# Optimization experiments

Hardware: AMD Instinct MI355X
Metric: run time of the kernel (lower is better)

Reference implementation:

```python
import jax, jax.numpy as jnp
import numpy as np

B, S, D, E = 4, 4096, 2048, 64
NOISE_STD = 1.0


def setup_inputs() -> dict:
    key = jax.random.key(0)
    k1, k2, k3, k4 = jax.random.split(key, 4)
    x = jax.random.normal(k1, (B, S, D), dtype=jnp.float32)
    lim = float(np.sqrt(6.0 / (D + E)))  # glorot_uniform
    W_gate = jax.random.uniform(k2, (D, E), jnp.float32, -lim, lim)
    # keras inits noise_dense kernel to zeros; use tiny random values so the
    # noise path is numerically exercised (zeros would make it trivially ln(2)).
    W_noise = 0.02 * jax.random.normal(k3, (D, E), dtype=jnp.float32)
    noise = jax.random.normal(k4, (B * S, E), dtype=jnp.float32)
    return {"x": x, "W_gate": W_gate, "W_noise": W_noise, "noise": noise, "top_k": 2}


def reference(x, W_gate, W_noise, noise, top_k):
    b, s, d = x.shape
    e = W_gate.shape[1]
    xf = x.reshape(-1, d)                         # [N, D], N = b*s
    gate_logits = xf @ W_gate                     # [N, E]
    # training-mode noise injection
    noise_logits = xf @ W_noise                   # [N, E]
    nstd = jax.nn.softplus(noise_logits) * (NOISE_STD / (e * e))
    gate_logits = gate_logits + noise * nstd
    # top-k mask + masked softmax
    top_vals, top_idx = jax.lax.top_k(gate_logits, top_k)   # [N, K]
    n = gate_logits.shape[0]
    mask = jnp.zeros_like(gate_logits).at[jnp.arange(n)[:, None], top_idx].set(1.0)
    masked_logits = jnp.where(mask > 0, gate_logits, jnp.float32(-1e9))
    expert_weights = jax.nn.softmax(masked_logits, axis=-1)  # [N, E]
    raw_gate_probs = jax.nn.softmax(gate_logits, axis=-1)    # [N, E]
    expert_weights = expert_weights.reshape(b, s, e)
    expert_indices = top_idx.reshape(b, s, top_k).astype(jnp.int32)
    return expert_weights, expert_indices, gate_logits, raw_gate_probs
```

## Files before the change

kernel.cpp:

```cpp
#include <hip/hip_runtime.h>
#include <math.h>


typedef _Float16 f16;
typedef f16  f16x4  __attribute__((ext_vector_type(4)));
typedef f16  f16x8  __attribute__((ext_vector_type(8)));
typedef float f32x16 __attribute__((ext_vector_type(16)));

constexpr int NROWS = 16384;
constexpr int DDIM  = 2048;
constexpr int NE    = 64;
constexpr int BM    = 32;
constexpr int KI    = 32;
constexpr float NSCALE = 1.0f / 4096.0f;

__device__ __forceinline__ int a_off(int buf, int h, int s, int v) {
    return (((buf * 2 + h) * 2 + s) * 2 + v) * 1024;
}

__device__ __forceinline__ float softplus_f(float x) {
    return fmaxf(x, 0.0f) + log1pf(expf(-fabsf(x)));
}

__global__ __launch_bounds__(256) void wprep_kernel(
    const float* __restrict__ Wg, const float* __restrict__ Wn,
    f16* __restrict__ ws)
{
    int t = blockIdx.x * 256 + threadIdx.x;
    int S = t >> 8;
    int f = (t >> 6) & 3;
    int l = t & 63;
    int k0  = S * 16 + (l >> 5) * 8;
    int col = f * 32 + (l & 31);
    const float* src = (col < NE) ? (Wg + col) : (Wn + col - NE);
    f16x8 hp, lp;
    #pragma unroll
    for (int j = 0; j < 8; ++j) {
        float w  = src[(size_t)(k0 + j) * NE];
        f16 h    = (f16)w;
        float hf = (float)h;
        hp[j] = h;
        lp[j] = (f16)((w - hf) * 64.0f);
    }
    size_t base = (size_t)(S * 4 + f) * 1024;
    *(f16x8*)(ws + base + l * 8)       = hp;
    *(f16x8*)(ws + base + 512 + l * 8) = lp;
}

__global__ __launch_bounds__(512, 4) void gemm_gating(
    const float* __restrict__ x, const f16* __restrict__ wfrag,
    const float* __restrict__ noise,
    float* __restrict__ out_w, float* __restrict__ out_idx,
    float* __restrict__ out_logits, float* __restrict__ out_probs)
{
    __shared__ __align__(16) char smem[49152];
    const int tid = threadIdx.x;
    const int l   = tid & 63;
    const int w   = tid >> 6;
    const int h   = w >> 2;
    const int f   = w & 3;
    const int row0 = blockIdx.x * BM;

    f32x16 acc1, acc2;
    #pragma unroll
    for (int r = 0; r < 16; ++r) { acc1[r] = 0.0f; acc2[r] = 0.0f; }

    const int h_s = w >> 2, s_s = (w >> 1) & 1, j4 = w & 1;
    const float* aSrc = x + (size_t)(row0 + (l & 31)) * DDIM
                          + h_s * 1024 + s_s * 16 + (l >> 5) * 8 + j4 * 4;
    auto loadA = [&](int t) -> float4 {
        return *(const float4*)(aSrc + (size_t)t * KI);
    };
    auto cvtWrite = [&](float4 xv, int buf) {
        float xs[4] = {xv.x, xv.y, xv.z, xv.w};
        f16x4 hi, lo;
        #pragma unroll
        for (int j = 0; j < 4; ++j) {
            f16 hh   = (f16)xs[j];
            float hf = (float)hh;
            hi[j] = hh;
            lo[j] = (f16)((xs[j] - hf) * 64.0f);
        }
        *(f16x4*)(smem + a_off(buf, h_s, s_s, 0) + l * 16 + j4 * 8) = hi;
        *(f16x4*)(smem + a_off(buf, h_s, s_s, 1) + l * 16 + j4 * 8) = lo;
    };

    const f16* bBase = wfrag + (size_t)f * 1024 + l * 8;
#define LOADB(t, H0, L0, H1, L1) do {                                       \
        const f16* _p = bBase + (size_t)(h * 64 + (t) * 2) * 4096;          \
        H0 = *(const f16x8*)_p;          L0 = *(const f16x8*)(_p + 512);    \
        H1 = *(const f16x8*)(_p + 4096); L1 = *(const f16x8*)(_p + 4608);   \
    } while (0)

    auto compute = [&](int buf, f16x8 Bh0, f16x8 Bl0, f16x8 Bh1, f16x8 Bl1) {
        #pragma unroll
        for (int s = 0; s < 2; ++s) {
            f16x8 Ah = *(const f16x8*)(smem + a_off(buf, h, s, 0) + l * 16);
            f16x8 Al = *(const f16x8*)(smem + a_off(buf, h, s, 1) + l * 16);
            f16x8 Bh = s ? Bh1 : Bh0;
            f16x8 Bl = s ? Bl1 : Bl0;
            acc1 = __builtin_amdgcn_mfma_f32_32x32x16_f16(Ah, Bh, acc1, 0, 0, 0);
            acc2 = __builtin_amdgcn_mfma_f32_32x32x16_f16(Ah, Bl, acc2, 0, 0, 0);
            acc2 = __builtin_amdgcn_mfma_f32_32x32x16_f16(Al, Bh, acc2, 0, 0, 0);
        }
    };

    float4 a0, a1, a2, a3;
    f16x8 b0h0, b0l0, b0h1, b0l1;
    f16x8 b1h0, b1l0, b1h1, b1l1;

    a0 = loadA(0); a1 = loadA(1); a2 = loadA(2); a3 = loadA(3);
    LOADB(0, b0h0, b0l0, b0h1, b0l1);
    LOADB(1, b1h0, b1l0, b1h1, b1l1);
    cvtWrite(a0, 0);
    cvtWrite(a1, 1);
    __syncthreads();

    for (int tb = 0; tb < 32; tb += 4) {
        compute(0, b0h0, b0l0, b0h1, b0l1);
        compute(1, b1h0, b1l0, b1h1, b1l1);
        if (tb + 4 < 32) { a0 = loadA(tb + 4); a1 = loadA(tb + 5); }
        if (tb + 2 < 32) {
            LOADB(tb + 2, b0h0, b0l0, b0h1, b0l1);
            LOADB(tb + 3, b1h0, b1l0, b1h1, b1l1);
        }
        cvtWrite(a2, 2);
        cvtWrite(a3, 3);
        __syncthreads();

        compute(2, b0h0, b0l0, b0h1, b0l1);
        compute(3, b1h0, b1l0, b1h1, b1l1);
        if (tb + 6 < 32) { a2 = loadA(tb + 6); a3 = loadA(tb + 7); }
        if (tb + 4 < 32) {
            LOADB(tb + 4, b0h0, b0l0, b0h1, b0l1);
            LOADB(tb + 5, b1h0, b1l0, b1h1, b1l1);
            cvtWrite(a0, 0);
            cvtWrite(a1, 1);
        }
        __syncthreads();
    }
#undef LOADB

    float* mg = (float*)(smem + 32768);
    if (h == 1) {
        #pragma unroll
        for (int r = 0; r < 16; ++r) {
            float cv = fmaf(acc2[r], 0.015625f, acc1[r]);
            int row = (r & 3) + 8 * (r >> 2) + 4 * (l >> 5);
            int col = f * 32 + (l & 31);
            mg[row * 128 + col] = cv;
        }
    }
    __syncthreads();

    float* lgf = (float*)smem;
    if (h == 0) {
        #pragma unroll
        for (int r = 0; r < 16; ++r) {
            float cv = fmaf(acc2[r], 0.015625f, acc1[r]);
            int row = (r & 3) + 8 * (r >> 2) + 4 * (l >> 5);
            int col = f * 32 + (l & 31);
            lgf[row * 132 + col] = cv + mg[row * 128 + col];
        }
    }
    __syncthreads();

    {
        const int pr = tid & 31;
        const int c4 = tid >> 5;
        const int n1 = row0 + pr;
        float4 G  = *(const float4*)(lgf + pr * 132 + c4 * 4);
        float4 NL = *(const float4*)(lgf + pr * 132 + 64 + c4 * 4);
        float4 NZ = *(const float4*)(noise + (size_t)n1 * NE + c4 * 4);
        G.x += NZ.x * softplus_f(NL.x) * NSCALE;
        G.y += NZ.y * softplus_f(NL.y) * NSCALE;
        G.z += NZ.z * softplus_f(NL.z) * NSCALE;
        G.w += NZ.w * softplus_f(NL.w) * NSCALE;
        *(float4*)(lgf + pr * 132 + c4 * 4) = G;
        *(float4*)(out_logits + (size_t)n1 * NE + c4 * 4) = G;
    }
    __syncthreads();

    if (w < 4) {
        const int g2   = l >> 3;
        const int c    = l & 7;
        const int row2 = w * 8 + g2;
        const int n2   = row0 + row2;

        float mv[8];
        {
            const float4* mr = (const float4*)(lgf + row2 * 132 + c * 8);
            float4 m0 = mr[0], m1 = mr[1];
            mv[0]=m0.x; mv[1]=m0.y; mv[2]=m0.z; mv[3]=m0.w;
            mv[4]=m1.x; mv[5]=m1.y; mv[6]=m1.z; mv[7]=m1.w;
        }
        float v0 = -INFINITY, v1 = -INFINITY;
        int i0 = 0, i1 = 0;
        #pragma unroll
        for (int j = 0; j < 8; ++j) {
            float v = mv[j]; int e = c * 8 + j;
            if (v > v0) { v1 = v0; i1 = i0; v0 = v; i0 = e; }
            else if (v > v1) { v1 = v; i1 = e; }
        }
        #pragma unroll
        for (int m = 1; m <= 4; m <<= 1) {
            float ov0 = __shfl_xor(v0, m), ov1 = __shfl_xor(v1, m);
            int   oi0 = __shfl_xor(i0, m), oi1 = __shfl_xor(i1, m);
            if (ov0 > v0) {
                bool keep = (v0 > ov1);
                v1 = keep ? v0 : ov1; i1 = keep ? i0 : oi1;
                v0 = ov0; i0 = oi0;
            } else if (ov0 > v1) {
                v1 = ov0; i1 = oi0;
            }
        }
        const int srcl = l & 56;
        v0 = __shfl(v0, srcl); i0 = __shfl(i0, srcl);
        v1 = __shfl(v1, srcl); i1 = __shfl(i1, srcl);

        float se = 0.0f;
        #pragma unroll
        for (int j = 0; j < 8; ++j) se += expf(mv[j] - v0);
        se += __shfl_xor(se, 1); se += __shfl_xor(se, 2); se += __shfl_xor(se, 4);
        float inv_se = 1.0f / se;

        float t  = expf(v1 - v0);
        float w0 = 1.0f / (1.0f + t);
        float w1 = t * w0;

        float pr[8], wt[8];
        #pragma unroll
        for (int j = 0; j < 8; ++j) {
            int e = c * 8 + j;
            pr[j] = expf(mv[j] - v0) * inv_se;
            wt[j] = (e == i0) ? w0 : ((e == i1) ? w1 : 0.0f);
        }
        *(float4*)(out_probs + (size_t)n2 * NE + c * 8)     = make_float4(pr[0], pr[1], pr[2], pr[3]);
        *(float4*)(out_probs + (size_t)n2 * NE + c * 8 + 4) = make_float4(pr[4], pr[5], pr[6], pr[7]);
        *(float4*)(out_w + (size_t)n2 * NE + c * 8)         = make_float4(wt[0], wt[1], wt[2], wt[3]);
        *(float4*)(out_w + (size_t)n2 * NE + c * 8 + 4)     = make_float4(wt[4], wt[5], wt[6], wt[7]);
        if (c == 0) {
            *(float2*)(out_idx + (size_t)n2 * 2) = make_float2((float)i0, (float)i1);
        }
    }
}

extern "C" void kernel_launch(void* const* d_in, const int* in_sizes, int n_in,
                              void* d_out, int out_size, void* d_ws, size_t ws_size,
                              hipStream_t stream) {
    (void)in_sizes; (void)n_in; (void)ws_size; (void)out_size;
    const float* x     = (const float*)d_in[0];
    const float* Wg    = (const float*)d_in[1];
    const float* Wn    = (const float*)d_in[2];
    const float* noise = (const float*)d_in[3];
    float* out        = (float*)d_out;
    float* out_w      = out;
    float* out_idx    = out + (size_t)NROWS * NE;
    float* out_logits = out_idx + (size_t)NROWS * 2;
    float* out_probs  = out_logits + (size_t)NROWS * NE;
    f16* wfrag = (f16*)d_ws;

    wprep_kernel<<<128, 256, 0, stream>>>(Wg, Wn, wfrag);
    gemm_gating<<<NROWS / BM, 512, 0, stream>>>(
        x, wfrag, noise, out_w, out_idx, out_logits, out_probs);
}
```

Before: 55.62 us.

## Split K across blocks with partial buffers and separate gating reduction kernel

Splits the GEMM's K dimension over a second grid dimension (4 or 2 splits, depending on workspace size), so more blocks are in flight. Each block writes fp32 partial logits to workspace, and a new reduce kernel sums the partials and then does the noise, top-k and softmax epilogue. The main loop also changes from two-buffer to one-buffer steps with more frequent barriers. This buys more parallelism at the cost of extra global traffic for the partials (up to 32MB written and read back), an extra launch, and more synchronisation.

```diff
diff --git a/kernel.cpp b/kernel.cpp
--- a/kernel.cpp
+++ b/kernel.cpp
@@ -11,7 +11,6 @@
 constexpr int DDIM  = 2048;
 constexpr int NE    = 64;
 constexpr int BM    = 32;
-constexpr int KI    = 32;
 constexpr float NSCALE = 1.0f / 4096.0f;
 
 __device__ __forceinline__ int a_off(int buf, int h, int s, int v) {
@@ -47,29 +46,31 @@
     *(f16x8*)(ws + base + 512 + l * 8) = lp;
 }
 
-__global__ __launch_bounds__(512, 4) void gemm_gating(
+template<int NSP>
+__global__ __launch_bounds__(512, 4) void gemm_phase1(
     const float* __restrict__ x, const f16* __restrict__ wfrag,
-    const float* __restrict__ noise,
-    float* __restrict__ out_w, float* __restrict__ out_idx,
-    float* __restrict__ out_logits, float* __restrict__ out_probs)
+    float* __restrict__ part)
 {
+    constexpr int SEGS = 1024 / (NSP * 32);
     __shared__ __align__(16) char smem[49152];
     const int tid = threadIdx.x;
     const int l   = tid & 63;
     const int w   = tid >> 6;
     const int h   = w >> 2;
     const int f   = w & 3;
+    const int sp  = blockIdx.y;
     const int row0 = blockIdx.x * BM;
+    const int k0 = sp * (DDIM / NSP);
 
     f32x16 acc1, acc2;
     #pragma unroll
     for (int r = 0; r < 16; ++r) { acc1[r] = 0.0f; acc2[r] = 0.0f; }
 
     const int h_s = w >> 2, s_s = (w >> 1) & 1, j4 = w & 1;
-    const float* aSrc = x + (size_t)(row0 + (l & 31)) * DDIM
-                          + h_s * 1024 + s_s * 16 + (l >> 5) * 8 + j4 * 4;
+    const float* aSrc = x + (size_t)(row0 + (l & 31)) * DDIM + k0
+                          + h_s * (SEGS * 32) + s_s * 16 + (l >> 5) * 8 + j4 * 4;
     auto loadA = [&](int t) -> float4 {
-        return *(const float4*)(aSrc + (size_t)t * KI);
+        return *(const float4*)(aSrc + (size_t)t * 32);
     };
     auto cvtWrite = [&](float4 xv, int buf) {
         float xs[4] = {xv.x, xv.y, xv.z, xv.w};
@@ -87,7 +88,8 @@
 
     const f16* bBase = wfrag + (size_t)f * 1024 + l * 8;
 #define LOADB(t, H0, L0, H1, L1) do {                                       \
-        const f16* _p = bBase + (size_t)(h * 64 + (t) * 2) * 4096;          \
+        const f16* _p = bBase + (size_t)(sp * (128 / NSP)                   \
+                                         + h * (SEGS * 2) + (t) * 2) * 4096;\
         H0 = *(const f16x8*)_p;          L0 = *(const f16x8*)(_p + 512);    \
         H1 = *(const f16x8*)(_p + 4096); L1 = *(const f16x8*)(_p + 4608);   \
     } while (0)
@@ -116,25 +118,31 @@
     cvtWrite(a1, 1);
     __syncthreads();
 
-    for (int tb = 0; tb < 32; tb += 4) {
+    for (int tb = 0; tb < SEGS; tb += 4) {
         compute(0, b0h0, b0l0, b0h1, b0l1);
+        if (tb + 4 < SEGS) a0 = loadA(tb + 4);
+        if (tb + 2 < SEGS) LOADB(tb + 2, b0h0, b0l0, b0h1, b0l1);
+        cvtWrite(a2, 2);
+        __syncthreads();
+
         compute(1, b1h0, b1l0, b1h1, b1l1);
-        if (tb + 4 < 32) { a0 = loadA(tb + 4); a1 = loadA(tb + 5); }
-        if (tb + 2 < 32) {
-            LOADB(tb + 2, b0h0, b0l0, b0h1, b0l1);
-            LOADB(tb + 3, b1h0, b1l0, b1h1, b1l1);
-        }
-        cvtWrite(a2, 2);
+        if (tb + 5 < SEGS) a1 = loadA(tb + 5);
+        if (tb + 3 < SEGS) LOADB(tb + 3, b1h0, b1l0, b1h1, b1l1);
         cvtWrite(a3, 3);
         __syncthreads();
 
         compute(2, b0h0, b0l0, b0h1, b0l1);
+        if (tb + 6 < SEGS) a2 = loadA(tb + 6);
+        if (tb + 4 < SEGS) {
+            LOADB(tb + 4, b0h0, b0l0, b0h1, b0l1);
+            cvtWrite(a0, 0);
+        }
+        __syncthreads();
+
         compute(3, b1h0, b1l0, b1h1, b1l1);
-        if (tb + 6 < 32) { a2 = loadA(tb + 6); a3 = loadA(tb + 7); }
-        if (tb + 4 < 32) {
-            LOADB(tb + 4, b0h0, b0l0, b0h1, b0l1);
+        if (tb + 7 < SEGS) a3 = loadA(tb + 7);
+        if (tb + 5 < SEGS) {
             LOADB(tb + 5, b1h0, b1l0, b1h1, b1l1);
-            cvtWrite(a0, 0);
             cvtWrite(a1, 1);
         }
         __syncthreads();
@@ -152,58 +160,91 @@
         }
     }
     __syncthreads();
-
-    float* lgf = (float*)smem;
     if (h == 0) {
         #pragma unroll
         for (int r = 0; r < 16; ++r) {
             float cv = fmaf(acc2[r], 0.015625f, acc1[r]);
             int row = (r & 3) + 8 * (r >> 2) + 4 * (l >> 5);
             int col = f * 32 + (l & 31);
-            lgf[row * 132 + col] = cv + mg[row * 128 + col];
-        }
+            part[((size_t)sp * NROWS + row0 + row) * 128 + col] = cv + mg[row * 128 + col];
+        }
+    }
+}
+
+template<int NSP>
+__global__ __launch_bounds__(256) void reduce_gating(
+    const float* __restrict__ part, const float* __restrict__ noise,
+    float* __restrict__ out_w, float* __restrict__ out_idx,
+    float* __restrict__ out_logits, float* __restrict__ out_probs)
+{
+    __shared__ float lgf[64 * 132];
+    const int tid = threadIdx.x;
+    const int l   = tid & 63;
+    const int w   = tid >> 6;
+    const int row0 = blockIdx.x * 64;
+
+    #pragma unroll
+    for (int q = 0; q < 8; ++q) {
+        int idx = q * 256 + tid;
+        int r   = idx >> 5;
+        int c4  = idx & 31;
+        float4 s = make_float4(0.f, 0.f, 0.f, 0.f);
+        #pragma unroll
+        for (int sp = 0; sp < NSP; ++sp) {
+            float4 v = *(const float4*)(part + ((size_t)sp * NROWS + row0 + r) * 128 + c4 * 4);
+            s.x += v.x; s.y += v.y; s.z += v.z; s.w += v.w;
+        }
+        *(float4*)(lgf + r * 132 + c4 * 4) = s;
     }
     __syncthreads();
 
     {
-        const int pr = tid & 31;
-        const int c4 = tid >> 5;
+        const int pr = tid & 63;
+        const int pc = tid >> 6;
         const int n1 = row0 + pr;
-        float4 G  = *(const float4*)(lgf + pr * 132 + c4 * 4);
-        float4 NL = *(const float4*)(lgf + pr * 132 + 64 + c4 * 4);
-        float4 NZ = *(const float4*)(noise + (size_t)n1 * NE + c4 * 4);
-        G.x += NZ.x * softplus_f(NL.x) * NSCALE;
-        G.y += NZ.y * softplus_f(NL.y) * NSCALE;
-        G.z += NZ.z * softplus_f(NL.z) * NSCALE;
-        G.w += NZ.w * softplus_f(NL.w) * NSCALE;
-        *(float4*)(lgf + pr * 132 + c4 * 4) = G;
-        *(float4*)(out_logits + (size_t)n1 * NE + c4 * 4) = G;
+        const float4* gl4 = (const float4*)(lgf + pr * 132 + pc * 16);
+        const float4* nl4 = (const float4*)(lgf + pr * 132 + 64 + pc * 16);
+        const float4* nz4 = (const float4*)(noise + (size_t)n1 * NE + pc * 16);
+        float4* gw4 = (float4*)(lgf + pr * 132 + pc * 16);
+        float4* ol4 = (float4*)(out_logits + (size_t)n1 * NE + pc * 16);
+        #pragma unroll
+        for (int q = 0; q < 4; ++q) {
+            float4 G = gl4[q], NL = nl4[q], NZ = nz4[q];
+            G.x += NZ.x * softplus_f(NL.x) * NSCALE;
+            G.y += NZ.y * softplus_f(NL.y) * NSCALE;
+            G.z += NZ.z * softplus_f(NL.z) * NSCALE;
+            G.w += NZ.w * softplus_f(NL.w) * NSCALE;
+            gw4[q] = G;
+            ol4[q] = G;
+        }
     }
     __syncthreads();
 
-    if (w < 4) {
-        const int g2   = l >> 3;
-        const int c    = l & 7;
-        const int row2 = w * 8 + g2;
+    {
+        const int g2   = l >> 2;
+        const int c    = l & 3;
+        const int row2 = w * 16 + g2;
         const int n2   = row0 + row2;
 
-        float mv[8];
+        float mv[16];
         {
-            const float4* mr = (const float4*)(lgf + row2 * 132 + c * 8);
-            float4 m0 = mr[0], m1 = mr[1];
-            mv[0]=m0.x; mv[1]=m0.y; mv[2]=m0.z; mv[3]=m0.w;
-            mv[4]=m1.x; mv[5]=m1.y; mv[6]=m1.z; mv[7]=m1.w;
+            const float4* mr = (const float4*)(lgf + row2 * 132 + c * 16);
+            #pragma unroll
+            for (int q = 0; q < 4; ++q) {
+                float4 v = mr[q];
+                mv[q*4+0] = v.x; mv[q*4+1] = v.y; mv[q*4+2] = v.z; mv[q*4+3] = v.w;
+            }
         }
         float v0 = -INFINITY, v1 = -INFINITY;
         int i0 = 0, i1 = 0;
         #pragma unroll
-        for (int j = 0; j < 8; ++j) {
-            float v = mv[j]; int e = c * 8 + j;
+        for (int j = 0; j < 16; ++j) {
+            float v = mv[j]; int e = c * 16 + j;
             if (v > v0) { v1 = v0; i1 = i0; v0 = v; i0 = e; }
             else if (v > v1) { v1 = v; i1 = e; }
         }
         #pragma unroll
-        for (int m = 1; m <= 4; m <<= 1) {
+        for (int m = 1; m <= 2; m <<= 1) {
             float ov0 = __shfl_xor(v0, m), ov1 = __shfl_xor(v1, m);
             int   oi0 = __shfl_xor(i0, m), oi1 = __shfl_xor(i1, m);
             if (ov0 > v0) {
@@ -214,31 +255,34 @@
                 v1 = ov0; i1 = oi0;
             }
         }
-        const int srcl = l & 56;
+        const int srcl = l & 60;
         v0 = __shfl(v0, srcl); i0 = __shfl(i0, srcl);
         v1 = __shfl(v1, srcl); i1 = __shfl(i1, srcl);
 
         float se = 0.0f;
         #pragma unroll
-        for (int j = 0; j < 8; ++j) se += expf(mv[j] - v0);
-        se += __shfl_xor(se, 1); se += __shfl_xor(se, 2); se += __shfl_xor(se, 4);
+        for (int j = 0; j < 16; ++j) se += expf(mv[j] - v0);
+        se += __shfl_xor(se, 1); se += __shfl_xor(se, 2);
         float inv_se = 1.0f / se;
 
         float t  = expf(v1 - v0);
         float w0 = 1.0f / (1.0f + t);
         float w1 = t * w0;
 
-        float pr[8], wt[8];
-        #pragma unroll
-        for (int j = 0; j < 8; ++j) {
-            int e = c * 8 + j;
+        float pr[16], wt[16];
+        #pragma unroll
+        for (int j = 0; j < 16; ++j) {
+            int e = c * 16 + j;
             pr[j] = expf(mv[j] - v0) * inv_se;
             wt[j] = (e == i0) ? w0 : ((e == i1) ? w1 : 0.0f);
         }
-        *(float4*)(out_probs + (size_t)n2 * NE + c * 8)     = make_float4(pr[0], pr[1], pr[2], pr[3]);
-        *(float4*)(out_probs + (size_t)n2 * NE + c * 8 + 4) = make_float4(pr[4], pr[5], pr[6], pr[7]);
-        *(float4*)(out_w + (size_t)n2 * NE + c * 8)         = make_float4(wt[0], wt[1], wt[2], wt[3]);
-        *(float4*)(out_w + (size_t)n2 * NE + c * 8 + 4)     = make_float4(wt[4], wt[5], wt[6], wt[7]);
+        #pragma unroll
+        for (int q = 0; q < 4; ++q) {
+            *(float4*)(out_probs + (size_t)n2 * NE + c * 16 + q * 4) =
+                make_float4(pr[q*4+0], pr[q*4+1], pr[q*4+2], pr[q*4+3]);
+            *(float4*)(out_w + (size_t)n2 * NE + c * 16 + q * 4) =
+                make_float4(wt[q*4+0], wt[q*4+1], wt[q*4+2], wt[q*4+3]);
+        }
         if (c == 0) {
             *(float2*)(out_idx + (size_t)n2 * 2) = make_float2((float)i0, (float)i1);
         }
@@ -248,7 +292,7 @@
 extern "C" void kernel_launch(void* const* d_in, const int* in_sizes, int n_in,
                               void* d_out, int out_size, void* d_ws, size_t ws_size,
                               hipStream_t stream) {
-    (void)in_sizes; (void)n_in; (void)ws_size; (void)out_size;
+    (void)in_sizes; (void)n_in; (void)out_size;
     const float* x     = (const float*)d_in[0];
     const float* Wg    = (const float*)d_in[1];
     const float* Wn    = (const float*)d_in[2];
@@ -258,9 +302,20 @@
     float* out_idx    = out + (size_t)NROWS * NE;
     float* out_logits = out_idx + (size_t)NROWS * 2;
     float* out_probs  = out_logits + (size_t)NROWS * NE;
-    f16* wfrag = (f16*)d_ws;
+
+    f16*   wfrag = (f16*)d_ws;
+    float* part  = (float*)((char*)d_ws + (1 << 20));
+    const size_t partBytes = (size_t)NROWS * 128 * 4;
 
     wprep_kernel<<<128, 256, 0, stream>>>(Wg, Wn, wfrag);
-    gemm_gating<<<NROWS / BM, 512, 0, stream>>>(
-        x, wfrag, noise, out_w, out_idx, out_logits, out_probs);
-}
+
+    if (ws_size >= (1u << 20) + 4 * partBytes) {
+        gemm_phase1<4><<<dim3(NROWS / BM, 4), 512, 0, stream>>>(x, wfrag, part);
+        reduce_gating<4><<<NROWS / 64, 256, 0, stream>>>(
+            part, noise, out_w, out_idx, out_logits, out_probs);
+    } else {
+        gemm_phase1<2><<<dim3(NROWS / BM, 2), 512, 0, stream>>>(x, wfrag, part);
+        reduce_gating<2><<<NROWS / 64, 256, 0, stream>>>(
+            part, noise, out_w, out_idx, out_logits, out_probs);
+    }
+}
```

Result: slower. 70.78 us (+27.2%).

## Stage A in 256-wide row-contiguous chunks with swizzled LDS and fewer barriers

Applied to the files above, without the earlier changes.

Each wave now loads four full rows of x with fully coalesced 1 KB-per-row float4 reads over 256-column super-steps, instead of scattered 16-byte pieces from 32 rows. The split-f16 A tile goes into a double-buffered 64 KB LDS area with an XOR-like slot swizzle to avoid bank conflicts, and the two K halves interleave within each super-step. This cuts barriers from two per 128 K to one per 256 K and should improve global load efficiency. In exchange LDS use rises from 48 KB to 64 KB, which may lower occupancy under the 4-block launch bound.

```diff
diff --git a/kernel.cpp b/kernel.cpp
--- a/kernel.cpp
+++ b/kernel.cpp
@@ -11,12 +11,9 @@
 constexpr int DDIM  = 2048;
 constexpr int NE    = 64;
 constexpr int BM    = 32;
-constexpr int KI    = 32;
+constexpr int SS    = 256;
+constexpr int NSS   = DDIM / SS;
 constexpr float NSCALE = 1.0f / 4096.0f;
-
-__device__ __forceinline__ int a_off(int buf, int h, int s, int v) {
-    return (((buf * 2 + h) * 2 + s) * 2 + v) * 1024;
-}
 
 __device__ __forceinline__ float softplus_f(float x) {
     return fmaxf(x, 0.0f) + log1pf(expf(-fabsf(x)));
@@ -53,7 +50,7 @@
     float* __restrict__ out_w, float* __restrict__ out_idx,
     float* __restrict__ out_logits, float* __restrict__ out_probs)
 {
-    __shared__ __align__(16) char smem[49152];
+    __shared__ __align__(16) char smem[65536];
     const int tid = threadIdx.x;
     const int l   = tid & 63;
     const int w   = tid >> 6;
@@ -65,80 +62,94 @@
     #pragma unroll
     for (int r = 0; r < 16; ++r) { acc1[r] = 0.0f; acc2[r] = 0.0f; }
 
-    const int h_s = w >> 2, s_s = (w >> 1) & 1, j4 = w & 1;
-    const float* aSrc = x + (size_t)(row0 + (l & 31)) * DDIM
-                          + h_s * 1024 + s_s * 16 + (l >> 5) * 8 + j4 * 4;
-    auto loadA = [&](int t) -> float4 {
-        return *(const float4*)(aSrc + (size_t)t * KI);
-    };
-    auto cvtWrite = [&](float4 xv, int buf) {
-        float xs[4] = {xv.x, xv.y, xv.z, xv.w};
-        f16x4 hi, lo;
-        #pragma unroll
-        for (int j = 0; j < 4; ++j) {
-            f16 hh   = (f16)xs[j];
-            float hf = (float)hh;
-            hi[j] = hh;
-            lo[j] = (f16)((xs[j] - hf) * 64.0f);
-        }
-        *(f16x4*)(smem + a_off(buf, h_s, s_s, 0) + l * 16 + j4 * 8) = hi;
-        *(f16x4*)(smem + a_off(buf, h_s, s_s, 1) + l * 16 + j4 * 8) = lo;
+    const int srow = w * 4;
+    const float* aSrc = x + (size_t)(row0 + srow) * DDIM + l * 4;
+    float4 av0, av1, av2, av3;
+    auto loadA = [&](int ss) {
+        const float* p = aSrc + ss * SS;
+        av0 = *(const float4*)(p);
+        av1 = *(const float4*)(p + DDIM);
+        av2 = *(const float4*)(p + 2 * DDIM);
+        av3 = *(const float4*)(p + 3 * DDIM);
+    };
+    auto cvtWrite = [&](int buf) {
+        float4 vv[4] = {av0, av1, av2, av3};
+        #pragma unroll
+        for (int i = 0; i < 4; ++i) {
+            int r = srow + i;
+            float xs[4] = {vv[i].x, vv[i].y, vv[i].z, vv[i].w};
+            f16x4 hi, lo;
+            #pragma unroll
+            for (int j = 0; j < 4; ++j) {
+                f16 hh   = (f16)xs[j];
+                float hf = (float)hh;
+                hi[j] = hh;
+                lo[j] = (f16)((xs[j] - hf) * 64.0f);
+            }
+            int slot = (l + 2 * r) & 63;
+            char* base = smem + buf * 32768 + r * 1024;
+            *(f16x4*)(base + slot * 8)       = hi;
+            *(f16x4*)(base + 512 + slot * 8) = lo;
+        }
+    };
+
+    const int R  = l & 31;
+    const int kg = l >> 5;
+    auto readA = [&](int buf, int T_loc, int s, f16x8& Ah, f16x8& Al) {
+        int ch   = T_loc * 8 + s * 4 + kg * 2;
+        int slot = (ch + 2 * R) & 63;
+        const char* base = smem + buf * 32768 + R * 1024;
+        Ah = *(const f16x8*)(base + slot * 8);
+        Al = *(const f16x8*)(base + 512 + slot * 8);
     };
 
     const f16* bBase = wfrag + (size_t)f * 1024 + l * 8;
-#define LOADB(t, H0, L0, H1, L1) do {                                       \
-        const f16* _p = bBase + (size_t)(h * 64 + (t) * 2) * 4096;          \
+#define LOADB(T, H0, L0, H1, L1) do {                                       \
+        const f16* _p = bBase + (size_t)(T) * 2 * 4096;                     \
         H0 = *(const f16x8*)_p;          L0 = *(const f16x8*)(_p + 512);    \
         H1 = *(const f16x8*)(_p + 4096); L1 = *(const f16x8*)(_p + 4608);   \
     } while (0)
 
-    auto compute = [&](int buf, f16x8 Bh0, f16x8 Bl0, f16x8 Bh1, f16x8 Bl1) {
-        #pragma unroll
-        for (int s = 0; s < 2; ++s) {
-            f16x8 Ah = *(const f16x8*)(smem + a_off(buf, h, s, 0) + l * 16);
-            f16x8 Al = *(const f16x8*)(smem + a_off(buf, h, s, 1) + l * 16);
-            f16x8 Bh = s ? Bh1 : Bh0;
-            f16x8 Bl = s ? Bl1 : Bl0;
-            acc1 = __builtin_amdgcn_mfma_f32_32x32x16_f16(Ah, Bh, acc1, 0, 0, 0);
-            acc2 = __builtin_amdgcn_mfma_f32_32x32x16_f16(Ah, Bl, acc2, 0, 0, 0);
-            acc2 = __builtin_amdgcn_mfma_f32_32x32x16_f16(Al, Bh, acc2, 0, 0, 0);
-        }
-    };
-
-    float4 a0, a1, a2, a3;
+    auto computeSub = [&](int buf, int T_loc,
+                          f16x8 Bh0, f16x8 Bl0, f16x8 Bh1, f16x8 Bl1) {
+        f16x8 Ah, Al;
+        readA(buf, T_loc, 0, Ah, Al);
+        acc1 = __builtin_amdgcn_mfma_f32_32x32x16_f16(Ah, Bh0, acc1, 0, 0, 0);
+        acc2 = __builtin_amdgcn_mfma_f32_32x32x16_f16(Ah, Bl0, acc2, 0, 0, 0);
+        acc2 = __builtin_amdgcn_mfma_f32_32x32x16_f16(Al, Bh0, acc2, 0, 0, 0);
+        readA(buf, T_loc, 1, Ah, Al);
+        acc1 = __builtin_amdgcn_mfma_f32_32x32x16_f16(Ah, Bh1, acc1, 0, 0, 0);
+        acc2 = __builtin_amdgcn_mfma_f32_32x32x16_f16(Ah, Bl1, acc2, 0, 0, 0);
+        acc2 = __builtin_amdgcn_mfma_f32_32x32x16_f16(Al, Bh1, acc2, 0, 0, 0);
+    };
+
     f16x8 b0h0, b0l0, b0h1, b0l1;
     f16x8 b1h0, b1l0, b1h1, b1l1;
 
-    a0 = loadA(0); a1 = loadA(1); a2 = loadA(2); a3 = loadA(3);
-    LOADB(0, b0h0, b0l0, b0h1, b0l1);
-    LOADB(1, b1h0, b1l0, b1h1, b1l1);
-    cvtWrite(a0, 0);
-    cvtWrite(a1, 1);
-    __syncthreads();
-
-    for (int tb = 0; tb < 32; tb += 4) {
-        compute(0, b0h0, b0l0, b0h1, b0l1);
-        compute(1, b1h0, b1l0, b1h1, b1l1);
-        if (tb + 4 < 32) { a0 = loadA(tb + 4); a1 = loadA(tb + 5); }
-        if (tb + 2 < 32) {
-            LOADB(tb + 2, b0h0, b0l0, b0h1, b0l1);
-            LOADB(tb + 3, b1h0, b1l0, b1h1, b1l1);
-        }
-        cvtWrite(a2, 2);
-        cvtWrite(a3, 3);
+    loadA(0);
+    LOADB(h * 4 + 0, b0h0, b0l0, b0h1, b0l1);
+    LOADB(h * 4 + 1, b1h0, b1l0, b1h1, b1l1);
+    cvtWrite(0);
+
+    for (int ss = 0; ss < NSS; ++ss) {
         __syncthreads();
-
-        compute(2, b0h0, b0l0, b0h1, b0l1);
-        compute(3, b1h0, b1l0, b1h1, b1l1);
-        if (tb + 6 < 32) { a2 = loadA(tb + 6); a3 = loadA(tb + 7); }
-        if (tb + 4 < 32) {
-            LOADB(tb + 4, b0h0, b0l0, b0h1, b0l1);
-            LOADB(tb + 5, b1h0, b1l0, b1h1, b1l1);
-            cvtWrite(a0, 0);
-            cvtWrite(a1, 1);
-        }
-        __syncthreads();
-    }
+        const int buf = ss & 1;
+        const int T0  = ss * 8 + h * 4;
+        if (ss + 1 < NSS) loadA(ss + 1);
+
+        computeSub(buf, h * 4 + 0, b0h0, b0l0, b0h1, b0l1);
+        LOADB(T0 + 2, b0h0, b0l0, b0h1, b0l1);
+        computeSub(buf, h * 4 + 1, b1h0, b1l0, b1h1, b1l1);
+        LOADB(T0 + 3, b1h0, b1l0, b1h1, b1l1);
+        computeSub(buf, h * 4 + 2, b0h0, b0l0, b0h1, b0l1);
+        if (ss + 1 < NSS) LOADB(T0 + 8, b0h0, b0l0, b0h1, b0l1);
+        computeSub(buf, h * 4 + 3, b1h0, b1l0, b1h1, b1l1);
+        if (ss + 1 < NSS) {
+            LOADB(T0 + 9, b1h0, b1l0, b1h1, b1l1);
+            cvtWrite(buf ^ 1);
+        }
+    }
+    __syncthreads();
 #undef LOADB
 
     float* mg = (float*)(smem + 32768);
```

After: 58.19 us. 4.6% more time.
